# Kernel tuning notes

Hardware: AMD Instinct MI355X
Metric: run time of the kernel (lower is better)

## Reference

```python
import jax, jax.numpy as jnp
import numpy as np

N, D, H = 1024, 256, 512


def _linear_init(key, fan_in, fan_out):
    kw, kb = jax.random.split(key)
    bound = 1.0 / np.sqrt(fan_in)
    w = jax.random.uniform(kw, (fan_in, fan_out), jnp.float32, -bound, bound)
    b = jax.random.uniform(kb, (fan_out,), jnp.float32, -bound, bound)
    return w, b


def setup_inputs() -> dict:
    key = jax.random.key(0)
    ks = jax.random.split(key, 8)
    domain_a = jax.random.normal(ks[0], (N, D), jnp.float32)
    domain_b = jax.random.normal(ks[1], (N, D), jnp.float32)
    mu_w0, mu_b0 = _linear_init(ks[2], D, H)
    mu_w1, mu_b1 = _linear_init(ks[3], H, H)
    mu_w2, mu_b2 = _linear_init(ks[4], H, D)
    lv_w0, lv_b0 = _linear_init(ks[5], D, H)
    lv_w1, lv_b1 = _linear_init(ks[6], H, H)
    lv_w2, lv_b2 = _linear_init(ks[7], H, D)
    return dict(domain_a=domain_a, domain_b=domain_b,
                mu_w0=mu_w0, mu_b0=mu_b0, mu_w1=mu_w1, mu_b1=mu_b1, mu_w2=mu_w2, mu_b2=mu_b2,
                lv_w0=lv_w0, lv_b0=lv_b0, lv_w1=lv_w1, lv_b1=lv_b1, lv_w2=lv_w2, lv_b2=lv_b2)


def _net(x, ws, bs, final_act):
    h = x
    for i in range(len(ws)):
        h = h @ ws[i] + bs[i]
        if i < len(ws) - 1:
            h = jax.nn.relu(h)
    return final_act(h)


def _l2norm(h):
    # L2NormEncoder == F.normalize(dim=-1), eps clamp like torch
    n = jnp.maximum(jnp.linalg.norm(h, axis=-1, keepdims=True), 1e-12)
    return h / n


def reference(domain_a, domain_b, mu_w0, mu_b0, mu_w1, mu_b1, mu_w2, mu_b2,
              lv_w0, lv_b0, lv_w1, lv_b1, lv_w2, lv_b2):
    mu_ws, mu_bs = [mu_w0, mu_w1, mu_w2], [mu_b0, mu_b1, mu_b2]
    lv_ws, lv_bs = [lv_w0, lv_w1, lv_w2], [lv_b0, lv_b1, lv_b2]

    # ---- embedding-model loss: prob-model params frozen (requires_grad=False) ----
    sg = jax.lax.stop_gradient
    mu = _net(domain_a, [sg(w) for w in mu_ws], [sg(b) for b in mu_bs], _l2norm)
    log_var = _net(domain_a, [sg(w) for w in lv_ws], [sg(b) for b in lv_bs], jnp.tanh)
    inv_var = jnp.exp(-log_var)                                  # [N, D]
    pos_probs = jnp.sum(-(domain_b - mu) ** 2 * inv_var - log_var, axis=-1)  # [N]
    # pairwise: [i, j, d] = b[j, d] - mu[i, d]; mean over j
    diff2_mean = jnp.mean((domain_b[None, :, :] - mu[:, None, :]) ** 2, axis=1)  # [N, D]
    neg_probs = jnp.sum(-diff2_mean * inv_var - log_var, axis=-1)  # [N]
    embed_model_loss = jnp.mean(pos_probs - neg_probs)

    # ---- prob-model loss: embeddings detached, params trainable ----
    a_d, b_d = sg(domain_a), sg(domain_b)
    mu2 = _net(a_d, mu_ws, mu_bs, _l2norm)
    lv2 = _net(a_d, lv_ws, lv_bs, jnp.tanh)
    prob_model_loss = jnp.mean(jnp.sum((b_d - mu2) ** 2 * jnp.exp(-lv2) + lv2, axis=-1))

    emb_coef, prob_coef = 1.0, 1.0
    loss = emb_coef * embed_model_loss + prob_coef * prob_model_loss
    return loss
```

## Files before the change

### kernel.cpp

```cpp
#include <hip/hip_runtime.h>
#include <hip/hip_fp16.h>

#define N_ROWS 1024
#define DIM 256
#define HID 512
#define CTR 16

typedef _Float16 half_t;
typedef __attribute__((ext_vector_type(4))) _Float16 half4v;
typedef __attribute__((ext_vector_type(8))) _Float16 half8v;
typedef __attribute__((ext_vector_type(16))) float f32x16;

struct Params {
    const float* a;
    const float* b;
    const float* w[6];
    const float* bias[6];
    unsigned* c1;
    unsigned* c2;
    unsigned* c3;
    float* acc;
    unsigned* done;
    float* ebsum;
    float* eb2sum;
    unsigned short* g_mu;
    unsigned short* g_lv;
    half_t* g_h1[2];
    half_t* g_h2[2];
    half_t* wt[6];
    float* out;
};

__global__ __launch_bounds__(256) void prep_kernel(Params p) {
    const int y = blockIdx.y, bx = blockIdx.x, tid = threadIdx.x;

    if (y == 6) {
        if (bx >= 64) return;
        const int d = tid, r0 = bx * 16;
        float s = 0.f, s2 = 0.f;
        #pragma unroll
        for (int r = 0; r < 16; ++r) {
            float v = p.b[(r0 + r) * DIM + d];
            s += v; s2 = fmaf(v, v, s2);
        }
        atomicAdd(&p.ebsum[d], s);
        atomicAdd(&p.eb2sum[d], s2);
        return;
    }
    __shared__ float T[32][33];
    const float* src = p.w[y];
    half_t* dst = p.wt[y];
    const int K = (y < 2) ? DIM : HID;
    const int N = (y < 4) ? HID : DIM;
    const int C = K >> 5;
    const int tilesN = N >> 5;
    if (bx >= C * tilesN) return;
    const int tk = bx / tilesN, tn = bx % tilesN;

    {
        const int r = tid >> 3, c4 = (tid & 7) * 4;
        float4 v = *(const float4*)&src[(tk * 32 + r) * N + tn * 32 + c4];
        T[r][c4 + 0] = v.x; T[r][c4 + 1] = v.y; T[r][c4 + 2] = v.z; T[r][c4 + 3] = v.w;
    }
    __syncthreads();
    const int which = tid >> 7;
    const int lane64 = (tid >> 1) & 63;
    const int epart = tid & 1;
    const int hi = lane64 >> 5, lr = lane64 & 31;
    const int rbase = which * 16 + hi * 8 + epart * 4;
    half4v h;
    h[0] = (half_t)T[rbase + 0][lr];
    h[1] = (half_t)T[rbase + 1][lr];
    h[2] = (half_t)T[rbase + 2][lr];
    h[3] = (half_t)T[rbase + 3][lr];
    *(half4v*)&dst[((tn * C + tk) * 2 + which) * 512 + lane64 * 8 + epart * 4] = h;
}

__device__ __forceinline__ void flag_add(unsigned* c) {
    asm volatile("s_waitcnt vmcnt(0)" ::: "memory");
    __syncthreads();
    if (threadIdx.x == 0)
        __hip_atomic_fetch_add(c, 1u, __ATOMIC_RELAXED, __HIP_MEMORY_SCOPE_AGENT);
}
__device__ __forceinline__ void flag_wait(unsigned* c, unsigned tgt) {
    if (threadIdx.x == 0) {
        while (__hip_atomic_load(c, __ATOMIC_RELAXED, __HIP_MEMORY_SCOPE_AGENT) < tgt)
            __builtin_amdgcn_s_sleep(1);
    }
    __syncthreads();
    asm volatile("" ::: "memory");
}

template <int KC>
__device__ __forceinline__ f32x16 mma_tile(const half_t* __restrict__ XA,
                                           const half_t* __restrict__ Wfrag,
                                           const int NCtot, const int tile,
                                           const int k0, const int lane) {
    const int lr = lane & 31, hi = lane >> 5;
    const int sa = (lr >> 3) & 3;
    const int aoff0 = lr * 40 + ((hi ^ sa) * 8);
    const int aoff1 = lr * 40 + (((hi + 2) ^ sa) * 8);
    const half_t* Wp = Wfrag + (tile * NCtot + k0) * 1024 + lane * 8;
    const half_t* Ap = XA + k0 * 1280;
    f32x16 acc;
    #pragma unroll
    for (int i = 0; i < 16; ++i) acc[i] = 0.f;
    #pragma unroll
    for (int c = 0; c < KC; ++c) {
        half8v av0 = *(const half8v*)&Ap[c * 1280 + aoff0];
        half8v av1 = *(const half8v*)&Ap[c * 1280 + aoff1];
        half8v bv0 = *(const half8v*)(Wp + c * 1024);
        half8v bv1 = *(const half8v*)(Wp + c * 1024 + 512);
        acc = __builtin_amdgcn_mfma_f32_32x32x16_f16(av0, bv0, acc, 0, 0, 0);
        acc = __builtin_amdgcn_mfma_f32_32x32x16_f16(av1, bv1, acc, 0, 0, 0);
    }
    return acc;
}

__device__ __forceinline__ void stage_a(const float* __restrict__ a, half_t* XA,
                                        const int R0, const int tid) {
    const int r = tid >> 4, q = tid & 15;
    const float* src = &a[(R0 + r) * DIM + q * 16];
    float4 v0 = *(const float4*)(src);
    float4 v1 = *(const float4*)(src + 4);
    float4 v2 = *(const float4*)(src + 8);
    float4 v3 = *(const float4*)(src + 12);
    half8v h0, h1;
    h0[0] = (half_t)v0.x; h0[1] = (half_t)v0.y; h0[2] = (half_t)v0.z; h0[3] = (half_t)v0.w;
    h0[4] = (half_t)v1.x; h0[5] = (half_t)v1.y; h0[6] = (half_t)v1.z; h0[7] = (half_t)v1.w;
    h1[0] = (half_t)v2.x; h1[1] = (half_t)v2.y; h1[2] = (half_t)v2.z; h1[3] = (half_t)v2.w;
    h1[4] = (half_t)v3.x; h1[5] = (half_t)v3.y; h1[6] = (half_t)v3.z; h1[7] = (half_t)v3.w;
    const int c = q >> 1, kb0 = (q & 1) * 2, sr = (r >> 3) & 3;
    *(half8v*)&XA[c * 1280 + r * 40 + ((kb0 ^ sr) * 8)] = h0;
    *(half8v*)&XA[c * 1280 + r * 40 + (((kb0 + 1) ^ sr) * 8)] = h1;
}

__device__ __forceinline__ void stage_h(const half_t* __restrict__ src, half_t* XA,
                                        const int R0, const int tid) {
    const int r = tid >> 4, q = tid & 15;
    const half_t* sp = &src[(R0 + r) * HID + q * 32];
    half8v x0 = *(const half8v*)(sp);
    half8v x1 = *(const half8v*)(sp + 8);
    half8v x2 = *(const half8v*)(sp + 16);
    half8v x3 = *(const half8v*)(sp + 24);
    const int sr = (r >> 3) & 3;
    half_t* d = &XA[q * 1280 + r * 40];
    *(half8v*)&d[(0 ^ sr) * 8] = x0;
    *(half8v*)&d[(1 ^ sr) * 8] = x1;
    *(half8v*)&d[(2 ^ sr) * 8] = x2;
    *(half8v*)&d[(3 ^ sr) * 8] = x3;
}

__device__ __forceinline__ void reduce2_store(f32x16 acc, float* red,
                                              const int tl, const int kh, const int lane,
                                              const float* __restrict__ bias, const int col0,
                                              unsigned short* __restrict__ dstG, const int Nout,
                                              const int R0, const bool relu) {
    __syncthreads();
    if (kh) {
        #pragma unroll
        for (int i = 0; i < 16; ++i) red[tl * 1024 + i * 64 + lane] = acc[i];
    }
    __syncthreads();
    if (!kh) {
        const int lr = lane & 31, hi = lane >> 5;
        const int col = col0 + lr;
        const float bv = bias[col];
        #pragma unroll
        for (int i = 0; i < 16; ++i) {
            float v = acc[i] + red[tl * 1024 + i * 64 + lane] + bv;
            if (relu) v = fmaxf(v, 0.f);
            const int row = (i & 3) + 8 * (i >> 2) + 4 * hi;
            union { half_t h; unsigned short u; } cv; cv.h = (half_t)v;
            __hip_atomic_store(&dstG[(R0 + row) * Nout + col], cv.u,
                               __ATOMIC_RELAXED, __HIP_MEMORY_SCOPE_AGENT);
        }
    }
}

__device__ __forceinline__ void reduce4_store(f32x16 acc, float* red,
                                              const int tl, const int kq, const int lane,
                                              const float* __restrict__ bias, const int col0,
                                              unsigned short* __restrict__ dstG, const int Nout,
                                              const int R0) {
    __syncthreads();
    if (kq) {
        #pragma unroll
        for (int i = 0; i < 16; ++i)
            red[(tl * 3 + kq - 1) * 1024 + i * 64 + lane] = acc[i];
    }
    __syncthreads();
    if (!kq) {
        const int lr = lane & 31, hi = lane >> 5;
        const int col = col0 + lr;
        const float bv = bias[col];
        #pragma unroll
        for (int i = 0; i < 16; ++i) {
            float v = acc[i] + bv
                    + red[(tl * 3 + 0) * 1024 + i * 64 + lane]
                    + red[(tl * 3 + 1) * 1024 + i * 64 + lane]
                    + red[(tl * 3 + 2) * 1024 + i * 64 + lane];
            const int row = (i & 3) + 8 * (i >> 2) + 4 * hi;
            union { half_t h; unsigned short u; } cv; cv.h = (half_t)v;
            __hip_atomic_store(&dstG[(R0 + row) * Nout + col], cv.u,
                               __ATOMIC_RELAXED, __HIP_MEMORY_SCOPE_AGENT);
        }
    }
}

__global__ void __launch_bounds__(512, 2) main_kernel(Params p) {
    __shared__ alignas(16) char smem[41024];
    half_t* XA = (half_t*)smem;
    float* red = (float*)smem;
    float* bsum = (float*)(smem + 40960);

    const int bid = blockIdx.x, tid = threadIdx.x;
    const int net = bid & 1, g = (bid >> 1) & 31, s = bid >> 6;
    const int R0 = g * 32;
    const int w = tid >> 6, lane = tid & 63;

    stage_a(p.a, XA, R0, tid);
    __syncthreads();
    {
        const int tl = w >> 1, kh = w & 1;
        const int tile = s * 4 + tl;
        f32x16 acc = mma_tile<4>(XA, p.wt[net], 8, tile, kh * 4, lane);
        reduce2_store(acc, red, tl, kh, lane, p.bias[net], tile * 32,
                      (unsigned short*)p.g_h1[net], HID, R0, true);
    }
    flag_add(p.c1 + (net * 32 + g) * CTR);

    flag_wait(p.c1 + (net * 32 + g) * CTR, 4);
    stage_h(p.g_h1[net], XA, R0, tid);
    __syncthreads();
    {
        const int tl = w >> 1, kh = w & 1;
        const int tile = s * 4 + tl;
        f32x16 acc = mma_tile<8>(XA, p.wt[2 + net], 16, tile, kh * 8, lane);
        reduce2_store(acc, red, tl, kh, lane, p.bias[2 + net], tile * 32,
                      (unsigned short*)p.g_h2[net], HID, R0, true);
    }
    flag_add(p.c2 + (net * 32 + g) * CTR);

    flag_wait(p.c2 + (net * 32 + g) * CTR, 4);
    stage_h(p.g_h2[net], XA, R0, tid);
    __syncthreads();
    {
        const int tl = w >> 2, kq = w & 3;
        const int tile = s * 2 + tl;
        f32x16 acc = mma_tile<4>(XA, p.wt[4 + net], 16, tile, kq * 4, lane);
        reduce4_store(acc, red, tl, kq, lane, p.bias[4 + net], tile * 32,
                      net ? p.g_lv : p.g_mu, DIM, R0);
    }
    flag_add(p.c3 + g * CTR);

    if (net == 0) return;

    if (tid == 0) *bsum = 0.f;
    flag_wait(p.c3 + g * CTR, 8);

    const int i = R0 + s * 8 + w;
    const int d0 = lane * 4;
    const half_t* muP = (const half_t*)p.g_mu;
    const half_t* lvP = (const half_t*)p.g_lv;
    half4v mh = *(const half4v*)&muP[i * DIM + d0];
    half4v lh = *(const half4v*)&lvP[i * DIM + d0];
    float4 ebf = *(const float4*)&p.ebsum[d0];
    float4 eb2f = *(const float4*)&p.eb2sum[d0];
    const float invN = 1.0f / (float)N_ROWS;
    float m4[4] = {(float)mh[0], (float)mh[1], (float)mh[2], (float)mh[3]};
    float l4[4] = {(float)lh[0], (float)lh[1], (float)lh[2], (float)lh[3]};
    float eb[4] = {ebf.x * invN, ebf.y * invN, ebf.z * invN, ebf.w * invN};
    float eb2[4] = {eb2f.x * invN, eb2f.y * invN, eb2f.z * invN, eb2f.w * invN};

    float ss = 0.f;
    #pragma unroll
    for (int t = 0; t < 4; ++t) ss = fmaf(m4[t], m4[t], ss);
    #pragma unroll
    for (int o = 32; o > 0; o >>= 1) ss += __shfl_xor(ss, o, 64);
    const float inv_norm = 1.f / fmaxf(sqrtf(ss), 1e-12f);

    float wacc = 0.f;
    #pragma unroll
    for (int t = 0; t < 4; ++t) {
        float mu = m4[t] * inv_norm;
        float lv = tanhf(l4[t]);
        float iv = expf(-lv);
        float diff2 = fmaf(mu, mu, fmaf(-2.f * mu, eb[t], eb2[t]));
        wacc += fmaf(diff2, iv, lv);
    }
    #pragma unroll
    for (int o = 32; o > 0; o >>= 1) wacc += __shfl_xor(wacc, o, 64);
    if (lane == 0) atomicAdd(bsum, wacc);
    __syncthreads();
    if (tid == 0) {
        atomicAdd(p.acc, *bsum);
        asm volatile("s_waitcnt vmcnt(0)" ::: "memory");
        unsigned prev = __hip_atomic_fetch_add(p.done, 1u, __ATOMIC_RELAXED,
                                               __HIP_MEMORY_SCOPE_AGENT);
        if (prev == 127u) {
            float v = __hip_atomic_load(p.acc, __ATOMIC_RELAXED, __HIP_MEMORY_SCOPE_AGENT);
            p.out[0] = v * (1.0f / (float)N_ROWS);
        }
    }
}

extern "C" void kernel_launch(void* const* d_in, const int* in_sizes, int n_in,
                              void* d_out, int out_size, void* d_ws, size_t ws_size,
                              hipStream_t stream) {
    Params p;
    p.a = (const float*)d_in[0];
    p.b = (const float*)d_in[1];
    p.w[0] = (const float*)d_in[2];  p.bias[0] = (const float*)d_in[3];
    p.w[2] = (const float*)d_in[4];  p.bias[2] = (const float*)d_in[5];
    p.w[4] = (const float*)d_in[6];  p.bias[4] = (const float*)d_in[7];
    p.w[1] = (const float*)d_in[8];  p.bias[1] = (const float*)d_in[9];
    p.w[3] = (const float*)d_in[10]; p.bias[3] = (const float*)d_in[11];
    p.w[5] = (const float*)d_in[12]; p.bias[5] = (const float*)d_in[13];

    float* f = (float*)d_ws;
    p.c1   = (unsigned*)f;
    p.c2   = (unsigned*)(f + 1024);
    p.c3   = (unsigned*)(f + 2048);
    p.acc  = f + 2560;
    p.done = (unsigned*)(f + 2576);
    p.ebsum  = f + 2816;
    p.eb2sum = f + 3072;
    p.g_mu = (unsigned short*)(f + 4096);
    p.g_lv = (unsigned short*)(f + 4096 + 65536 * 2);
    half_t* hb = (half_t*)(f + 4096 + 65536 * 4);
    p.g_h1[0] = hb;  hb += N_ROWS * HID;
    p.g_h1[1] = hb;  hb += N_ROWS * HID;
    p.g_h2[0] = hb;  hb += N_ROWS * HID;
    p.g_h2[1] = hb;  hb += N_ROWS * HID;
    p.wt[0] = hb;  hb += HID * DIM;
    p.wt[1] = hb;  hb += HID * DIM;
    p.wt[2] = hb;  hb += HID * HID;
    p.wt[3] = hb;  hb += HID * HID;
    p.wt[4] = hb;  hb += DIM * HID;
    p.wt[5] = hb;  hb += DIM * HID;
    p.out = (float*)d_out;

    hipMemsetAsync(d_ws, 0, 16384, stream);
    prep_kernel<<<dim3(256, 7), 256, 0, stream>>>(p);
    main_kernel<<<256, 512, 0, stream>>>(p);
}
```

Baseline: 31.17 us.

## Load MFMA A-operands directly from global and stage outputs for wide stores

Removes the LDS staging of activations (stage_a/stage_h plus a barrier per layer). Each wave now loads its A fragments straight from global memory, with software-prefetched register double/quad buffering of A and W fragments. Layer outputs are first gathered in LDS as fp16 tiles, then written to global with coalesced 64-bit atomic stores instead of scattered 16-bit stores. The ebsum loads are hoisted before the flag wait. The cost is redundant global/L2 reads of A across waves and an extra barrier in each reduction step.

```diff
diff --git a/kernel.cpp b/kernel.cpp
--- a/kernel.cpp
+++ b/kernel.cpp
@@ -92,181 +92,205 @@
 }
 
 template <int KC>
-__device__ __forceinline__ f32x16 mma_tile(const half_t* __restrict__ XA,
-                                           const half_t* __restrict__ Wfrag,
-                                           const int NCtot, const int tile,
-                                           const int k0, const int lane) {
-    const int lr = lane & 31, hi = lane >> 5;
-    const int sa = (lr >> 3) & 3;
-    const int aoff0 = lr * 40 + ((hi ^ sa) * 8);
-    const int aoff1 = lr * 40 + (((hi + 2) ^ sa) * 8);
-    const half_t* Wp = Wfrag + (tile * NCtot + k0) * 1024 + lane * 8;
-    const half_t* Ap = XA + k0 * 1280;
+__device__ __forceinline__ f32x16 mma_h(const half_t* __restrict__ Ap,
+                                        const half_t* __restrict__ Wp) {
     f32x16 acc;
     #pragma unroll
     for (int i = 0; i < 16; ++i) acc[i] = 0.f;
+    half8v ab[4][2], wb[4][2];
+    #define ISS(c) do {                                          \
+        ab[(c) & 3][0] = *(const half8v*)(Ap + (c) * 32);        \
+        ab[(c) & 3][1] = *(const half8v*)(Ap + (c) * 32 + 16);   \
+        wb[(c) & 3][0] = *(const half8v*)(Wp + (c) * 1024);      \
+        wb[(c) & 3][1] = *(const half8v*)(Wp + (c) * 1024 + 512);\
+    } while (0)
+    #pragma unroll
+    for (int c = 0; c < 4 && c < KC; ++c) ISS(c);
     #pragma unroll
     for (int c = 0; c < KC; ++c) {
-        half8v av0 = *(const half8v*)&Ap[c * 1280 + aoff0];
-        half8v av1 = *(const half8v*)&Ap[c * 1280 + aoff1];
-        half8v bv0 = *(const half8v*)(Wp + c * 1024);
-        half8v bv1 = *(const half8v*)(Wp + c * 1024 + 512);
-        acc = __builtin_amdgcn_mfma_f32_32x32x16_f16(av0, bv0, acc, 0, 0, 0);
-        acc = __builtin_amdgcn_mfma_f32_32x32x16_f16(av1, bv1, acc, 0, 0, 0);
-    }
+        half8v a0 = ab[c & 3][0], a1 = ab[c & 3][1];
+        half8v b0 = wb[c & 3][0], b1 = wb[c & 3][1];
+        if (c + 4 < KC) ISS(c + 4);
+        acc = __builtin_amdgcn_mfma_f32_32x32x16_f16(a0, b0, acc, 0, 0, 0);
+        acc = __builtin_amdgcn_mfma_f32_32x32x16_f16(a1, b1, acc, 0, 0, 0);
+    }
+    #undef ISS
     return acc;
 }
 
-__device__ __forceinline__ void stage_a(const float* __restrict__ a, half_t* XA,
-                                        const int R0, const int tid) {
-    const int r = tid >> 4, q = tid & 15;
-    const float* src = &a[(R0 + r) * DIM + q * 16];
-    float4 v0 = *(const float4*)(src);
-    float4 v1 = *(const float4*)(src + 4);
-    float4 v2 = *(const float4*)(src + 8);
-    float4 v3 = *(const float4*)(src + 12);
-    half8v h0, h1;
-    h0[0] = (half_t)v0.x; h0[1] = (half_t)v0.y; h0[2] = (half_t)v0.z; h0[3] = (half_t)v0.w;
-    h0[4] = (half_t)v1.x; h0[5] = (half_t)v1.y; h0[6] = (half_t)v1.z; h0[7] = (half_t)v1.w;
-    h1[0] = (half_t)v2.x; h1[1] = (half_t)v2.y; h1[2] = (half_t)v2.z; h1[3] = (half_t)v2.w;
-    h1[4] = (half_t)v3.x; h1[5] = (half_t)v3.y; h1[6] = (half_t)v3.z; h1[7] = (half_t)v3.w;
-    const int c = q >> 1, kb0 = (q & 1) * 2, sr = (r >> 3) & 3;
-    *(half8v*)&XA[c * 1280 + r * 40 + ((kb0 ^ sr) * 8)] = h0;
-    *(half8v*)&XA[c * 1280 + r * 40 + (((kb0 + 1) ^ sr) * 8)] = h1;
-}
-
-__device__ __forceinline__ void stage_h(const half_t* __restrict__ src, half_t* XA,
-                                        const int R0, const int tid) {
-    const int r = tid >> 4, q = tid & 15;
-    const half_t* sp = &src[(R0 + r) * HID + q * 32];
-    half8v x0 = *(const half8v*)(sp);
-    half8v x1 = *(const half8v*)(sp + 8);
-    half8v x2 = *(const half8v*)(sp + 16);
-    half8v x3 = *(const half8v*)(sp + 24);
-    const int sr = (r >> 3) & 3;
-    half_t* d = &XA[q * 1280 + r * 40];
-    *(half8v*)&d[(0 ^ sr) * 8] = x0;
-    *(half8v*)&d[(1 ^ sr) * 8] = x1;
-    *(half8v*)&d[(2 ^ sr) * 8] = x2;
-    *(half8v*)&d[(3 ^ sr) * 8] = x3;
-}
-
-__device__ __forceinline__ void reduce2_store(f32x16 acc, float* red,
-                                              const int tl, const int kh, const int lane,
-                                              const float* __restrict__ bias, const int col0,
-                                              unsigned short* __restrict__ dstG, const int Nout,
-                                              const int R0, const bool relu) {
+template <int KC>
+__device__ __forceinline__ f32x16 mma_a32(const float* __restrict__ Ap,
+                                          const half_t* __restrict__ Wp) {
+    f32x16 acc;
+    #pragma unroll
+    for (int i = 0; i < 16; ++i) acc[i] = 0.f;
+    float4 af[2][4];
+    half8v wb[4][2];
+    #define ISSA(c) do {                                         \
+        af[(c) & 1][0] = *(const float4*)(Ap + (c) * 32);        \
+        af[(c) & 1][1] = *(const float4*)(Ap + (c) * 32 + 4);    \
+        af[(c) & 1][2] = *(const float4*)(Ap + (c) * 32 + 16);   \
+        af[(c) & 1][3] = *(const float4*)(Ap + (c) * 32 + 20);   \
+    } while (0)
+    #define ISSW(c) do {                                         \
+        wb[(c) & 3][0] = *(const half8v*)(Wp + (c) * 1024);      \
+        wb[(c) & 3][1] = *(const half8v*)(Wp + (c) * 1024 + 512);\
+    } while (0)
+    ISSA(0);
+    if (KC > 1) ISSA(1);
+    #pragma unroll
+    for (int c = 0; c < 4 && c < KC; ++c) ISSW(c);
+    #pragma unroll
+    for (int c = 0; c < KC; ++c) {
+        float4 x0 = af[c & 1][0], x1 = af[c & 1][1];
+        float4 x2 = af[c & 1][2], x3 = af[c & 1][3];
+        if (c + 2 < KC) ISSA(c + 2);
+        half8v a0, a1;
+        a0[0] = (half_t)x0.x; a0[1] = (half_t)x0.y; a0[2] = (half_t)x0.z; a0[3] = (half_t)x0.w;
+        a0[4] = (half_t)x1.x; a0[5] = (half_t)x1.y; a0[6] = (half_t)x1.z; a0[7] = (half_t)x1.w;
+        a1[0] = (half_t)x2.x; a1[1] = (half_t)x2.y; a1[2] = (half_t)x2.z; a1[3] = (half_t)x2.w;
+        a1[4] = (half_t)x3.x; a1[5] = (half_t)x3.y; a1[6] = (half_t)x3.z; a1[7] = (half_t)x3.w;
+        half8v b0 = wb[c & 3][0], b1 = wb[c & 3][1];
+        if (c + 4 < KC) ISSW(c + 4);
+        acc = __builtin_amdgcn_mfma_f32_32x32x16_f16(a0, b0, acc, 0, 0, 0);
+        acc = __builtin_amdgcn_mfma_f32_32x32x16_f16(a1, b1, acc, 0, 0, 0);
+    }
+    #undef ISSA
+    #undef ISSW
+    return acc;
+}
+
+__device__ __forceinline__ void reduce2_wide(f32x16 acc, char* smem, int tl, int kh,
+                                             int lane, int tid,
+                                             const float* __restrict__ bias, int colbase,
+                                             unsigned short* __restrict__ dstG, int Nout,
+                                             int R0, bool relu) {
+    float* redf = (float*)smem;
+    half_t* redh = (half_t*)(smem + 24576);
     __syncthreads();
     if (kh) {
         #pragma unroll
-        for (int i = 0; i < 16; ++i) red[tl * 1024 + i * 64 + lane] = acc[i];
+        for (int i = 0; i < 16; ++i) redf[tl * 1024 + i * 64 + lane] = acc[i];
     }
     __syncthreads();
     if (!kh) {
         const int lr = lane & 31, hi = lane >> 5;
-        const int col = col0 + lr;
-        const float bv = bias[col];
+        const int coll = tl * 32 + lr;
+        const float bv = bias[colbase + coll];
         #pragma unroll
         for (int i = 0; i < 16; ++i) {
-            float v = acc[i] + red[tl * 1024 + i * 64 + lane] + bv;
+            float v = acc[i] + redf[tl * 1024 + i * 64 + lane] + bv;
             if (relu) v = fmaxf(v, 0.f);
             const int row = (i & 3) + 8 * (i >> 2) + 4 * hi;
-            union { half_t h; unsigned short u; } cv; cv.h = (half_t)v;
-            __hip_atomic_store(&dstG[(R0 + row) * Nout + col], cv.u,
-                               __ATOMIC_RELAXED, __HIP_MEMORY_SCOPE_AGENT);
+            redh[row * 136 + coll] = (half_t)v;
         }
     }
-}
-
-__device__ __forceinline__ void reduce4_store(f32x16 acc, float* red,
-                                              const int tl, const int kq, const int lane,
-                                              const float* __restrict__ bias, const int col0,
-                                              unsigned short* __restrict__ dstG, const int Nout,
-                                              const int R0) {
+    __syncthreads();
+    {
+        const int row = tid >> 4, c8 = (tid & 15) * 8;
+        const unsigned long long* sp = (const unsigned long long*)&redh[row * 136 + c8];
+        unsigned long long v0 = sp[0], v1 = sp[1];
+        unsigned long long* dp = (unsigned long long*)&dstG[(R0 + row) * Nout + colbase + c8];
+        __hip_atomic_store(dp, v0, __ATOMIC_RELAXED, __HIP_MEMORY_SCOPE_AGENT);
+        __hip_atomic_store(dp + 1, v1, __ATOMIC_RELAXED, __HIP_MEMORY_SCOPE_AGENT);
+    }
+}
+
+__device__ __forceinline__ void reduce4_wide(f32x16 acc, char* smem, int tl, int kq,
+                                             int lane, int tid,
+                                             const float* __restrict__ bias, int colbase,
+                                             unsigned short* __restrict__ dstG, int Nout,
+                                             int R0) {
+    float* redf = (float*)smem;
+    half_t* redh = (half_t*)(smem + 24576);
     __syncthreads();
     if (kq) {
         #pragma unroll
         for (int i = 0; i < 16; ++i)
-            red[(tl * 3 + kq - 1) * 1024 + i * 64 + lane] = acc[i];
+            redf[(tl * 3 + kq - 1) * 1024 + i * 64 + lane] = acc[i];
     }
     __syncthreads();
     if (!kq) {
         const int lr = lane & 31, hi = lane >> 5;
-        const int col = col0 + lr;
-        const float bv = bias[col];
+        const int coll = tl * 32 + lr;
+        const float bv = bias[colbase + coll];
         #pragma unroll
         for (int i = 0; i < 16; ++i) {
             float v = acc[i] + bv
-                    + red[(tl * 3 + 0) * 1024 + i * 64 + lane]
-                    + red[(tl * 3 + 1) * 1024 + i * 64 + lane]
-                    + red[(tl * 3 + 2) * 1024 + i * 64 + lane];
+                    + redf[(tl * 3 + 0) * 1024 + i * 64 + lane]
+                    + redf[(tl * 3 + 1) * 1024 + i * 64 + lane]
+                    + redf[(tl * 3 + 2) * 1024 + i * 64 + lane];
             const int row = (i & 3) + 8 * (i >> 2) + 4 * hi;
-            union { half_t h; unsigned short u; } cv; cv.h = (half_t)v;
-            __hip_atomic_store(&dstG[(R0 + row) * Nout + col], cv.u,
-                               __ATOMIC_RELAXED, __HIP_MEMORY_SCOPE_AGENT);
+            redh[row * 72 + coll] = (half_t)v;
         }
     }
+    __syncthreads();
+    {
+        const int row = tid >> 4, c4 = (tid & 15) * 4;
+        unsigned long long v0 = *(const unsigned long long*)&redh[row * 72 + c4];
+        unsigned long long* dp = (unsigned long long*)&dstG[(R0 + row) * Nout + colbase + c4];
+        __hip_atomic_store(dp, v0, __ATOMIC_RELAXED, __HIP_MEMORY_SCOPE_AGENT);
+    }
 }
 
 __global__ void __launch_bounds__(512, 2) main_kernel(Params p) {
-    __shared__ alignas(16) char smem[41024];
-    half_t* XA = (half_t*)smem;
-    float* red = (float*)smem;
-    float* bsum = (float*)(smem + 40960);
+    __shared__ alignas(16) char smem[33344];
+    float* bsum = (float*)(smem + 33280);
 
     const int bid = blockIdx.x, tid = threadIdx.x;
     const int net = bid & 1, g = (bid >> 1) & 31, s = bid >> 6;
     const int R0 = g * 32;
     const int w = tid >> 6, lane = tid & 63;
-
-    stage_a(p.a, XA, R0, tid);
-    __syncthreads();
+    const int lr = lane & 31, hi = lane >> 5;
+
     {
         const int tl = w >> 1, kh = w & 1;
         const int tile = s * 4 + tl;
-        f32x16 acc = mma_tile<4>(XA, p.wt[net], 8, tile, kh * 4, lane);
-        reduce2_store(acc, red, tl, kh, lane, p.bias[net], tile * 32,
-                      (unsigned short*)p.g_h1[net], HID, R0, true);
+        const float* Ap = p.a + (R0 + lr) * DIM + kh * 128 + hi * 8;
+        const half_t* Wp = p.wt[net] + (tile * 8 + kh * 4) * 1024 + lane * 8;
+        f32x16 acc = mma_a32<4>(Ap, Wp);
+        reduce2_wide(acc, smem, tl, kh, lane, tid, p.bias[net], s * 128,
+                     (unsigned short*)p.g_h1[net], HID, R0, true);
     }
     flag_add(p.c1 + (net * 32 + g) * CTR);
 
     flag_wait(p.c1 + (net * 32 + g) * CTR, 4);
-    stage_h(p.g_h1[net], XA, R0, tid);
-    __syncthreads();
     {
         const int tl = w >> 1, kh = w & 1;
         const int tile = s * 4 + tl;
-        f32x16 acc = mma_tile<8>(XA, p.wt[2 + net], 16, tile, kh * 8, lane);
-        reduce2_store(acc, red, tl, kh, lane, p.bias[2 + net], tile * 32,
-                      (unsigned short*)p.g_h2[net], HID, R0, true);
+        const half_t* Ap = p.g_h1[net] + (R0 + lr) * HID + kh * 256 + hi * 8;
+        const half_t* Wp = p.wt[2 + net] + (tile * 16 + kh * 8) * 1024 + lane * 8;
+        f32x16 acc = mma_h<8>(Ap, Wp);
+        reduce2_wide(acc, smem, tl, kh, lane, tid, p.bias[2 + net], s * 128,
+                     (unsigned short*)p.g_h2[net], HID, R0, true);
     }
     flag_add(p.c2 + (net * 32 + g) * CTR);
 
     flag_wait(p.c2 + (net * 32 + g) * CTR, 4);
-    stage_h(p.g_h2[net], XA, R0, tid);
-    __syncthreads();
     {
         const int tl = w >> 2, kq = w & 3;
         const int tile = s * 2 + tl;
-        f32x16 acc = mma_tile<4>(XA, p.wt[4 + net], 16, tile, kq * 4, lane);
-        reduce4_store(acc, red, tl, kq, lane, p.bias[4 + net], tile * 32,
-                      net ? p.g_lv : p.g_mu, DIM, R0);
+        const half_t* Ap = p.g_h2[net] + (R0 + lr) * HID + kq * 128 + hi * 8;
+        const half_t* Wp = p.wt[4 + net] + (tile * 16 + kq * 4) * 1024 + lane * 8;
+        f32x16 acc = mma_h<4>(Ap, Wp);
+        reduce4_wide(acc, smem, tl, kq, lane, tid, p.bias[4 + net], s * 64,
+                     net ? p.g_lv : p.g_mu, DIM, R0);
     }
     flag_add(p.c3 + g * CTR);
 
     if (net == 0) return;
 
     if (tid == 0) *bsum = 0.f;
+    const int d0 = lane * 4;
+    float4 ebf = *(const float4*)&p.ebsum[d0];
+    float4 eb2f = *(const float4*)&p.eb2sum[d0];
     flag_wait(p.c3 + g * CTR, 8);
 
     const int i = R0 + s * 8 + w;
-    const int d0 = lane * 4;
     const half_t* muP = (const half_t*)p.g_mu;
     const half_t* lvP = (const half_t*)p.g_lv;
     half4v mh = *(const half4v*)&muP[i * DIM + d0];
     half4v lh = *(const half4v*)&lvP[i * DIM + d0];
-    float4 ebf = *(const float4*)&p.ebsum[d0];
-    float4 eb2f = *(const float4*)&p.eb2sum[d0];
     const float invN = 1.0f / (float)N_ROWS;
     float m4[4] = {(float)mh[0], (float)mh[1], (float)mh[2], (float)mh[3]};
     float l4[4] = {(float)lh[0], (float)lh[1], (float)lh[2], (float)lh[3]};
```

Result: slower. 36.75 us (+17.9%).
